# Performance work log

Measured on AMD Instinct MI355X. Metric: run time of the kernel, lower is better.

## Reference

```python
import jax, jax.numpy as jnp
import numpy as np

E = 128   # embedding_dim
H = 8     # num_attention_heads
D = 16    # head_size = E // H


def setup_inputs() -> dict:
    key = jax.random.key(0)
    ks = jax.random.split(key, 7)
    B, N = 2, 512
    x = jax.random.normal(ks[0], (B, N, E), jnp.float32)
    e = jax.random.uniform(ks[1], (B, N, N), jnp.float32)  # dense pairwise edge weights
    s_qkv = 1.0 / np.sqrt(D)
    w_qkv = jax.random.uniform(ks[2], (3 * H * D, E), jnp.float32, -s_qkv, s_qkv)
    w_ekv = jax.random.normal(ks[3], (2 * H * D, 1), jnp.float32) * 1.0
    b_ekv = jax.random.normal(ks[4], (2 * H * D,), jnp.float32) * 0.01
    s_prj = 1.0 / np.sqrt(E)
    w_prj = jax.random.uniform(ks[5], (E, H * D), jnp.float32, -s_prj, s_prj)
    b_prj = jnp.zeros((E,), jnp.float32)
    return {"x": x, "e": e, "w_qkv": w_qkv, "w_ekv": w_ekv,
            "b_ekv": b_ekv, "w_prj": w_prj, "b_prj": b_prj}


def reference(x, e, w_qkv, w_ekv, b_ekv, w_prj, b_prj):
    B, N, _ = x.shape
    # qkv projection: [B,N,3*H*D] split per einops '(S H D)'
    qkv = (x @ w_qkv.T).reshape(B, N, 3, H, D)
    q = jnp.transpose(qkv[:, :, 0], (0, 2, 1, 3))  # [B,H,N,D]
    k = jnp.transpose(qkv[:, :, 1], (0, 2, 1, 3))  # [B,H,N,D]
    v = jnp.transpose(qkv[:, :, 2], (0, 2, 1, 3))  # [B,H,N,D]
    # edge-conditioned K/V biases: Linear(1 -> 2HD) + LeakyReLU(0.01)
    ekv = jax.nn.leaky_relu(e[..., None] * w_ekv[:, 0] + b_ekv)  # [B,N,M,2HD]
    ekv = ekv.reshape(B, N, N, 2, H, D)
    ekm = jnp.transpose(ekv[..., 0, :, :], (0, 3, 1, 2, 4))  # [B,H,N,M,D]
    evm = jnp.transpose(ekv[..., 1, :, :], (0, 3, 1, 2, 4))  # [B,H,N,M,D]
    # dots[b,h,n,m] = q[b,h,n] . (k[b,h,n] + ekm[b,h,n,m])
    # NOTE: original uses the key of the *query* node n (broadcast over m).
    dots = jnp.sum(q * k, axis=-1)[..., None] \
        + jnp.einsum('bhnd,bhnmd->bhnm', q, ekm)
    attn = jax.nn.softmax(dots / np.sqrt(D), axis=-1)  # [B,H,N,M]
    # hat[b,h,n] = sum_m attn * (v[b,h,n] + evm[b,h,n,m])
    hat = v * jnp.sum(attn, axis=-1)[..., None] \
        + jnp.einsum('bhnm,bhnmd->bhnd', attn, evm)  # [B,H,N,D]
    out = jnp.transpose(hat, (0, 2, 1, 3)).reshape(B, N, H * D) @ w_prj.T + b_prj
    return out
```

## Files before the change

kernel.cpp:

```cpp
#include <hip/hip_runtime.h>
#include <math.h>

#define BATCH 2
#define NSEQ  512
#define EDIM  128
#define HNUM  8
#define DDIM  16
#define MROWS (BATCH*NSEQ)

__global__ __launch_bounds__(256)
void qv_gemm(const float* __restrict__ x, const float* __restrict__ w,
             float* __restrict__ qv) {
    __shared__ float4 As[32 * 32];
    __shared__ float4 Bs[64 * 32];

    const int tid  = threadIdx.x;
    const int row0 = blockIdx.y * 32;
    const int bx   = blockIdx.x;
    const int wr0  = (bx >> 1) * 256 + (bx & 1) * 64;
    const int cc0  = (bx >> 1) * 128 + (bx & 1) * 64;

    #pragma unroll
    for (int it = 0; it < 4; ++it) {
        int idx = tid + it * 256;
        int r = idx >> 5, k4 = idx & 31;
        As[r * 32 + (k4 ^ ((r >> 2) & 7))] =
            ((const float4*)(x + (size_t)(row0 + r) * 128))[k4];
    }
    #pragma unroll
    for (int it = 0; it < 8; ++it) {
        int idx = tid + it * 256;
        int r = idx >> 5, k4 = idx & 31;
        Bs[r * 32 + (k4 ^ ((r >> 2) & 7))] =
            ((const float4*)(w + (size_t)(wr0 + r) * 128))[k4];
    }
    __syncthreads();

    const int ty  = tid >> 4;
    const int tx  = tid & 15;
    const int ra  = ty * 2;
    const int swa = (ra >> 2) & 7;
    const int rb  = tx * 4;
    const int swb = tx & 7;

    float acc[2][4] = {};
    #pragma unroll
    for (int k4 = 0; k4 < 32; ++k4) {
        float4 a0 = As[ ra      * 32 + (k4 ^ swa)];
        float4 a1 = As[(ra + 1) * 32 + (k4 ^ swa)];
        float4 bv4[4];
        #pragma unroll
        for (int j = 0; j < 4; ++j)
            bv4[j] = Bs[(rb + j) * 32 + (k4 ^ swb)];
        #pragma unroll
        for (int j = 0; j < 4; ++j) {
            acc[0][j] = fmaf(a0.x, bv4[j].x, acc[0][j]);
            acc[0][j] = fmaf(a0.y, bv4[j].y, acc[0][j]);
            acc[0][j] = fmaf(a0.z, bv4[j].z, acc[0][j]);
            acc[0][j] = fmaf(a0.w, bv4[j].w, acc[0][j]);
            acc[1][j] = fmaf(a1.x, bv4[j].x, acc[1][j]);
            acc[1][j] = fmaf(a1.y, bv4[j].y, acc[1][j]);
            acc[1][j] = fmaf(a1.z, bv4[j].z, acc[1][j]);
            acc[1][j] = fmaf(a1.w, bv4[j].w, acc[1][j]);
        }
    }

    #pragma unroll
    for (int i = 0; i < 2; ++i) {
        float* crow = qv + (size_t)(row0 + ra + i) * 256 + cc0 + rb;
        *(float4*)crow = make_float4(acc[i][0], acc[i][1], acc[i][2], acc[i][3]);
    }
}

__global__ __launch_bounds__(512)
void attn_proj(const float* __restrict__ qv,   const float* __restrict__ e,
               const float* __restrict__ wekv, const float* __restrict__ bekv,
               const float* __restrict__ wprj, const float* __restrict__ bprj,
               float* __restrict__ out) {
    __shared__ float hat_s[EDIM];
    __shared__ float red[HNUM][DDIM][65];

    const int tid  = threadIdx.x;
    const int lane = tid & 63;
    const int h    = __builtin_amdgcn_readfirstlane(tid >> 6);
    const int bn   = blockIdx.x;

    const float* qrow = qv + (size_t)bn * 256 + h * DDIM;
    const float* vrow = qrow + 128;
    const float* erow = e + (size_t)bn * NSEQ;

    const float SC = 0.25f * 1.44269504088896340736f;

    float wk[DDIM], bk[DDIM], cd[DDIM], wvv[DDIM], bv[DDIM];
    float qwk = 0.f;
    #pragma unroll
    for (int d = 0; d < DDIM; ++d) {
        float q = qrow[d];
        wk[d]  = wekv[h * DDIM + d];
        bk[d]  = bekv[h * DDIM + d];
        wvv[d] = wekv[EDIM + h * DDIM + d];
        bv[d]  = bekv[EDIM + h * DDIM + d];
        qwk    = fmaf(q, wk[d], qwk);
        cd[d]  = 0.495f * SC * q;
    }
    const float Alin = SC * 0.505f * qwk;

    float4 e0 = ((const float4*)erow)[lane];
    float4 e1 = ((const float4*)erow)[lane + 64];
    float evs[8] = {e0.x, e0.y, e0.z, e0.w, e1.x, e1.y, e1.z, e1.w};

    float racc[DDIM];
    #pragma unroll
    for (int d = 0; d < DDIM; ++d) racc[d] = 0.f;
    float sp = 0.f, spe = 0.f;
    #pragma unroll
    for (int c = 0; c < 8; ++c) {
        float s = evs[c];
        float dot = s * Alin;
        #pragma unroll
        for (int d = 0; d < DDIM; ++d) {
            float t = fmaf(s, wk[d], bk[d]);
            dot = fmaf(cd[d], fabsf(t), dot);
        }
        float p = __builtin_amdgcn_exp2f(dot);
        sp  += p;
        spe  = fmaf(p, s, spe);
        #pragma unroll
        for (int d = 0; d < DDIM; ++d) {
            float t = fmaf(s, wvv[d], bv[d]);
            racc[d] = fmaf(p, fabsf(t), racc[d]);
        }
    }

    #pragma unroll
    for (int off = 1; off < 64; off <<= 1) {
        sp  += __shfl_xor(sp,  off, 64);
        spe += __shfl_xor(spe, off, 64);
    }

    #pragma unroll
    for (int d = 0; d < DDIM; ++d)
        red[h][d][lane] = racc[d];
    __syncthreads();
    const int rc = lane & 15, rg = lane >> 4;
    float part = 0.f;
    #pragma unroll
    for (int j = 0; j < 16; ++j)
        part += red[h][rc][rg * 16 + j];
    part += __shfl_xor(part, 16, 64);
    part += __shfl_xor(part, 32, 64);

    if (lane < DDIM) {
        float wvs = wekv[EDIM + h * DDIM + lane];
        float bvs = bekv[EDIM + h * DDIM + lane];
        float acc = 0.495f * part + 0.505f * fmaf(wvs, spe, bvs * sp);
        hat_s[h * DDIM + lane] = vrow[lane] + acc / sp;
    }
    __syncthreads();

    const int c    = tid >> 2;
    const int quad = tid & 3;
    const float4* wp = (const float4*)(wprj + (size_t)c * EDIM + quad * 32);
    const float4* hp = (const float4*)(hat_s + quad * 32);
    float s = 0.f;
    #pragma unroll
    for (int j = 0; j < 8; ++j) {
        float4 w4 = wp[j], h4 = hp[j];
        s = fmaf(w4.x, h4.x, s);
        s = fmaf(w4.y, h4.y, s);
        s = fmaf(w4.z, h4.z, s);
        s = fmaf(w4.w, h4.w, s);
    }
    s += __shfl_xor(s, 1, 64);
    s += __shfl_xor(s, 2, 64);
    if (quad == 0)
        out[(size_t)bn * EDIM + c] = s + bprj[c];
}

extern "C" void kernel_launch(void* const* d_in, const int* in_sizes, int n_in,
                              void* d_out, int out_size, void* d_ws, size_t ws_size,
                              hipStream_t stream) {
    const float* x     = (const float*)d_in[0];
    const float* e     = (const float*)d_in[1];
    const float* w_qkv = (const float*)d_in[2];
    const float* w_ekv = (const float*)d_in[3];
    const float* b_ekv = (const float*)d_in[4];
    const float* w_prj = (const float*)d_in[5];
    const float* b_prj = (const float*)d_in[6];
    float* out = (float*)d_out;

    float* qv = (float*)d_ws;

    qv_gemm<<<dim3(4, MROWS / 32), 256, 0, stream>>>(x, w_qkv, qv);

    attn_proj<<<MROWS, 512, 0, stream>>>(qv, e, w_ekv, b_ekv, w_prj, b_prj, out);
}
```

Measured before the change: 90.84 us.

## Process two query rows per block and reuse projection weights across them

```diff
diff --git a/kernel.cpp b/kernel.cpp
--- a/kernel.cpp
+++ b/kernel.cpp
@@ -72,22 +72,28 @@
     }
 }
 
-__global__ __launch_bounds__(512)
+__global__ __launch_bounds__(1024)
 void attn_proj(const float* __restrict__ qv,   const float* __restrict__ e,
                const float* __restrict__ wekv, const float* __restrict__ bekv,
                const float* __restrict__ wprj, const float* __restrict__ bprj,
                float* __restrict__ out) {
-    __shared__ float hat_s[EDIM];
-    __shared__ float red[HNUM][DDIM][65];
+    __shared__ float hat_s[2][EDIM];
+    __shared__ float red[16][DDIM][65];
 
     const int tid  = threadIdx.x;
     const int lane = tid & 63;
-    const int h    = __builtin_amdgcn_readfirstlane(tid >> 6);
-    const int bn   = blockIdx.x;
+    const int wv   = tid >> 6;
+    const int h    = __builtin_amdgcn_readfirstlane(wv & 7);
+    const int r    = __builtin_amdgcn_readfirstlane(wv >> 3);
+    const int bn   = blockIdx.x * 2 + r;
+
+    const float* erow = e + (size_t)bn * NSEQ;
+    float4 e0 = ((const float4*)erow)[lane];
+    float4 e1 = ((const float4*)erow)[lane + 64];
+    float evs[8] = {e0.x, e0.y, e0.z, e0.w, e1.x, e1.y, e1.z, e1.w};
 
     const float* qrow = qv + (size_t)bn * 256 + h * DDIM;
     const float* vrow = qrow + 128;
-    const float* erow = e + (size_t)bn * NSEQ;
 
     const float SC = 0.25f * 1.44269504088896340736f;
 
@@ -105,10 +111,6 @@
     }
     const float Alin = SC * 0.505f * qwk;
 
-    float4 e0 = ((const float4*)erow)[lane];
-    float4 e1 = ((const float4*)erow)[lane + 64];
-    float evs[8] = {e0.x, e0.y, e0.z, e0.w, e1.x, e1.y, e1.z, e1.w};
-
     float racc[DDIM];
     #pragma unroll
     for (int d = 0; d < DDIM; ++d) racc[d] = 0.f;
@@ -132,6 +134,13 @@
         }
     }
 
+    const int oc  = tid >> 3;
+    const int seg = tid & 7;
+    const float4* wp = (const float4*)(wprj + (size_t)oc * EDIM + seg * 16);
+    float4 w4[4];
+    #pragma unroll
+    for (int j = 0; j < 4; ++j) w4[j] = wp[j];
+
     #pragma unroll
     for (int off = 1; off < 64; off <<= 1) {
         sp  += __shfl_xor(sp,  off, 64);
@@ -140,13 +149,12 @@
 
     #pragma unroll
     for (int d = 0; d < DDIM; ++d)
-        red[h][d][lane] = racc[d];
-    __syncthreads();
+        red[wv][d][lane] = racc[d];
     const int rc = lane & 15, rg = lane >> 4;
     float part = 0.f;
     #pragma unroll
     for (int j = 0; j < 16; ++j)
-        part += red[h][rc][rg * 16 + j];
+        part += red[wv][rc][rg * 16 + j];
     part += __shfl_xor(part, 16, 64);
     part += __shfl_xor(part, 32, 64);
 
@@ -154,27 +162,30 @@
         float wvs = wekv[EDIM + h * DDIM + lane];
         float bvs = bekv[EDIM + h * DDIM + lane];
         float acc = 0.495f * part + 0.505f * fmaf(wvs, spe, bvs * sp);
-        hat_s[h * DDIM + lane] = vrow[lane] + acc / sp;
+        hat_s[r][h * DDIM + lane] = vrow[lane] + acc / sp;
     }
     __syncthreads();
 
-    const int c    = tid >> 2;
-    const int quad = tid & 3;
-    const float4* wp = (const float4*)(wprj + (size_t)c * EDIM + quad * 32);
-    const float4* hp = (const float4*)(hat_s + quad * 32);
-    float s = 0.f;
-    #pragma unroll
-    for (int j = 0; j < 8; ++j) {
-        float4 w4 = wp[j], h4 = hp[j];
-        s = fmaf(w4.x, h4.x, s);
-        s = fmaf(w4.y, h4.y, s);
-        s = fmaf(w4.z, h4.z, s);
-        s = fmaf(w4.w, h4.w, s);
-    }
-    s += __shfl_xor(s, 1, 64);
-    s += __shfl_xor(s, 2, 64);
-    if (quad == 0)
-        out[(size_t)bn * EDIM + c] = s + bprj[c];
+    const float4* h0 = (const float4*)(&hat_s[0][seg * 16]);
+    const float4* h1 = (const float4*)(&hat_s[1][seg * 16]);
+    float s0 = 0.f, s1 = 0.f;
+    #pragma unroll
+    for (int j = 0; j < 4; ++j) {
+        float4 a = w4[j], p0 = h0[j], p1 = h1[j];
+        s0 = fmaf(a.x, p0.x, s0); s0 = fmaf(a.y, p0.y, s0);
+        s0 = fmaf(a.z, p0.z, s0); s0 = fmaf(a.w, p0.w, s0);
+        s1 = fmaf(a.x, p1.x, s1); s1 = fmaf(a.y, p1.y, s1);
+        s1 = fmaf(a.z, p1.z, s1); s1 = fmaf(a.w, p1.w, s1);
+    }
+    #pragma unroll
+    for (int off = 1; off < 8; off <<= 1) {
+        s0 += __shfl_xor(s0, off, 64);
+        s1 += __shfl_xor(s1, off, 64);
+    }
+    if (seg < 2) {
+        float v = (seg ? s1 : s0) + bprj[oc];
+        out[(size_t)(blockIdx.x * 2 + seg) * EDIM + oc] = v;
+    }
 }
 
 extern "C" void kernel_launch(void* const* d_in, const int* in_sizes, int n_in,
@@ -193,5 +204,6 @@
 
     qv_gemm<<<dim3(4, MROWS / 32), 256, 0, stream>>>(x, w_qkv, qv);
 
-    attn_proj<<<MROWS, 512, 0, stream>>>(qv, e, w_ekv, b_ekv, w_prj, b_prj, out);
+    attn_proj<<<MROWS / 2, 1024, 0, stream>>>(qv, e, w_ekv, b_ekv,
+                                              w_prj, b_prj, out);
 }
```

New measurement: 84.99 us. 6.4% less time.
